# Optimization experiments

Hardware: AMD Instinct MI355X
Metric: run time of the kernel (lower is better)

Reference implementation:

```python
import jax, jax.numpy as jnp
import numpy as np

B, IN_DIM, HID = 4096, 1024, 1024


def _linear(x, W, b):
    # torch nn.Linear: y = x @ W.T + b, W is [out, in]
    return x @ W.T + b


def setup_inputs() -> dict:
    key = jax.random.key(0)
    ks = jax.random.split(key, 15)
    s_in = 1.0 / np.sqrt(IN_DIM + HID)
    s_x = 1.0 / np.sqrt(IN_DIM)
    s_h = 1.0 / np.sqrt(HID)
    return {
        "x": jax.random.normal(ks[0], (B, IN_DIM), jnp.float32),
        "h_prev": jax.random.normal(ks[1], (B, HID), jnp.float32),
        "c_prev": jax.random.normal(ks[2], (B, HID), jnp.float32),
        "Wi": jax.random.normal(ks[3], (HID, IN_DIM + HID), jnp.float32) * s_in,
        "bi": jax.random.normal(ks[4], (HID,), jnp.float32) * s_in,
        "Wf": jax.random.normal(ks[5], (HID, IN_DIM + HID), jnp.float32) * s_in,
        "bf": jax.random.normal(ks[6], (HID,), jnp.float32) * s_in,
        "Wo": jax.random.normal(ks[7], (HID, IN_DIM + HID), jnp.float32) * s_in,
        "bo": jax.random.normal(ks[8], (HID,), jnp.float32) * s_in,
        "Wxs": jax.random.normal(ks[9], (HID, IN_DIM), jnp.float32) * s_x,
        "bxs": jax.random.normal(ks[10], (HID,), jnp.float32) * s_x,
        "Wxg": jax.random.normal(ks[11], (HID, IN_DIM), jnp.float32) * s_x,
        "bxg": jax.random.normal(ks[12], (HID,), jnp.float32) * s_x,
        "Whg": jax.random.normal(ks[13], (HID, HID), jnp.float32) * s_h,
        "bhg": jax.random.normal(ks[14], (HID,), jnp.float32) * s_h,
    }


def reference(x, h_prev, c_prev, Wi, bi, Wf, bf, Wo, bo, Wxs, bxs, Wxg, bxg, Whg, bhg):
    # Fuse the three (in_dim+hid)->hid gate GEMMs into one concatenated GEMM.
    concat = jnp.concatenate([x, h_prev], axis=-1)          # [B, in_dim+hid]
    W_ifo = jnp.concatenate([Wi, Wf, Wo], axis=0)           # [3*hid, in_dim+hid]
    b_ifo = jnp.concatenate([bi, bf, bo], axis=0)           # [3*hid]
    gates = jax.nn.sigmoid(_linear(concat, W_ifo, b_ifo))   # [B, 3*hid]
    i_t, f_t, o_t = jnp.split(gates, 3, axis=-1)
    s_t = _linear(x, Wxs, bxs)
    cand_lin = _linear(x, Wxg, bxg) + _linear(h_prev, Whg, bhg)
    g_t = jnp.tanh(s_t * cand_lin)
    # refined=False branch
    c_t = f_t * c_prev + i_t * g_t
    h_t = o_t * jnp.tanh(c_t)
    return (h_t, c_t)
```

## Files before the change

kernel.cpp:

```cpp
#include <hip/hip_runtime.h>

typedef unsigned short u16;
typedef __attribute__((ext_vector_type(8))) __bf16 bf16x8;
typedef __attribute__((ext_vector_type(4))) float f32x4;
typedef __attribute__((ext_vector_type(4))) unsigned short u16x4;

#define AS1 __attribute__((address_space(1)))
#define AS3 __attribute__((address_space(3)))

#define OB_X    0L
#define OB_H    4194304L
#define OB_WI   8388608L
#define OB_WF   10485760L
#define OB_WO   12582912L
#define OB_WXS  14680064L
#define OB_WXG  15728640L
#define OB_WHG  16777216L
#define BLOB_EL 17825792L

__device__ __forceinline__ u16 f2b(float f) {
    unsigned u = __float_as_uint(f);
    u += 0x7fffu + ((u >> 16) & 1u);
    return (u16)(u >> 16);
}

__global__ __launch_bounds__(256) void convert_all(
    const float* __restrict__ x, const float* __restrict__ h,
    const float* __restrict__ Wi, const float* __restrict__ Wf,
    const float* __restrict__ Wo, const float* __restrict__ Wxs,
    const float* __restrict__ Wxg, const float* __restrict__ Whg,
    u16* __restrict__ blob)
{
    long e = ((long)blockIdx.x * 256 + threadIdx.x) * 8;
    const float* src; long off;
    if      (e < OB_H)   { src = x;   off = e; }
    else if (e < OB_WI)  { src = h;   off = e - OB_H; }
    else if (e < OB_WF)  { src = Wi;  off = e - OB_WI; }
    else if (e < OB_WO)  { src = Wf;  off = e - OB_WF; }
    else if (e < OB_WXS) { src = Wo;  off = e - OB_WO; }
    else if (e < OB_WXG) { src = Wxs; off = e - OB_WXS; }
    else if (e < OB_WHG) { src = Wxg; off = e - OB_WXG; }
    else                 { src = Whg; off = e - OB_WHG; }
    f32x4 v0 = *(const f32x4*)(src + off);
    f32x4 v1 = *(const f32x4*)(src + off + 4);
    u16x4 o0, o1;
    o0.x = f2b(v0.x); o0.y = f2b(v0.y); o0.z = f2b(v0.z); o0.w = f2b(v0.w);
    o1.x = f2b(v1.x); o1.y = f2b(v1.y); o1.z = f2b(v1.z); o1.w = f2b(v1.w);
    *(u16x4*)(blob + e) = o0;
    *(u16x4*)(blob + e + 4) = o1;
}

__device__ __forceinline__ void stageB(u16* dst, const u16* src, int ld,
                                       int t, int er, int gsw) {
    __builtin_amdgcn_global_load_lds(
        (AS1 void*)(src + er * ld + gsw),
        (AS3 void*)(dst + t * 8), 16, 0, 0);
}

__device__ __forceinline__ float sigf(float z) {
    return 1.f / (1.f + __expf(-z));
}

__global__ __launch_bounds__(512, 2) void srulstm_fused(
    const u16* __restrict__ blob,
    const float* __restrict__ c_prev,
    const float* __restrict__ bi, const float* __restrict__ bfv,
    const float* __restrict__ bo, const float* __restrict__ bxs,
    const float* __restrict__ bxg, const float* __restrict__ bhg,
    float* __restrict__ out)
{
    __shared__ __align__(16) u16 As[128 * 64];
    __shared__ __align__(16) u16 Bs[5 * 64 * 64];

    const u16* x   = blob + OB_X;
    const u16* h   = blob + OB_H;

    const int t = threadIdx.x;
    const int j0 = blockIdx.x * 64;
    const int m0 = blockIdx.y * 128;

    const u16* w0   = blob + OB_WI  + j0 * 2048;
    const u16* w1   = blob + OB_WF  + j0 * 2048;
    const u16* w2   = blob + OB_WO  + j0 * 2048;
    const u16* w3lo = blob + OB_WXG + j0 * 1024;
    const u16* w3hi = blob + OB_WHG + j0 * 1024;
    const u16* w4   = blob + OB_WXS + j0 * 1024;

    const u16* aLo = x + m0 * 1024;
    const u16* aHi = h + m0 * 1024;

    const int lane = t & 63;
    const int wave = t >> 6;
    const int wm = (wave >> 1) << 5;
    const int wn = (wave & 1) << 5;
    const int fr = lane & 15;
    const int fq = lane >> 4;
    const int r7 = fr & 7;

    f32x4 acc[5][2][2] = {};

    const int er = t >> 3;
    const int gsw = (((t & 7) ^ (er & 7)) << 3);

    for (int k0 = 0; k0 < 2048; k0 += 64) {
        const u16* aSrc = ((k0 < 1024) ? aLo : aHi) + (k0 & 1023);
#pragma unroll
        for (int it = 0; it < 2; ++it) {
            const int row = it * 64 + er;
            __builtin_amdgcn_global_load_lds(
                (AS1 void*)(aSrc + row * 1024 + gsw),
                (AS3 void*)(As + (it * 512 + t) * 8), 16, 0, 0);
        }
        stageB(Bs,         w0 + k0, 2048, t, er, gsw);
        stageB(Bs + 4096,  w1 + k0, 2048, t, er, gsw);
        stageB(Bs + 8192,  w2 + k0, 2048, t, er, gsw);
        stageB(Bs + 12288, (k0 < 1024) ? (w3lo + k0) : (w3hi + (k0 - 1024)),
               1024, t, er, gsw);
        if (k0 < 1024)
            stageB(Bs + 16384, w4 + k0, 1024, t, er, gsw);
        __syncthreads();
#pragma unroll
        for (int kk = 0; kk < 64; kk += 32) {
            const int sw = ((((kk >> 3) + fq) ^ r7) << 3);
            bf16x8 a[2];
#pragma unroll
            for (int mi = 0; mi < 2; ++mi)
                a[mi] = *(const bf16x8*)(As + (wm + mi * 16 + fr) * 64 + sw);
#pragma unroll
            for (int s = 0; s < 4; ++s) {
                bf16x8 b0 = *(const bf16x8*)(Bs + s * 4096 + (wn + fr) * 64 + sw);
                bf16x8 b1 = *(const bf16x8*)(Bs + s * 4096 + (wn + 16 + fr) * 64 + sw);
#pragma unroll
                for (int mi = 0; mi < 2; ++mi) {
                    acc[s][mi][0] = __builtin_amdgcn_mfma_f32_16x16x32_bf16(
                        a[mi], b0, acc[s][mi][0], 0, 0, 0);
                    acc[s][mi][1] = __builtin_amdgcn_mfma_f32_16x16x32_bf16(
                        a[mi], b1, acc[s][mi][1], 0, 0, 0);
                }
            }
            if (k0 < 1024) {
                bf16x8 b0 = *(const bf16x8*)(Bs + 16384 + (wn + fr) * 64 + sw);
                bf16x8 b1 = *(const bf16x8*)(Bs + 16384 + (wn + 16 + fr) * 64 + sw);
#pragma unroll
                for (int mi = 0; mi < 2; ++mi) {
                    acc[4][mi][0] = __builtin_amdgcn_mfma_f32_16x16x32_bf16(
                        a[mi], b0, acc[4][mi][0], 0, 0, 0);
                    acc[4][mi][1] = __builtin_amdgcn_mfma_f32_16x16x32_bf16(
                        a[mi], b1, acc[4][mi][1], 0, 0, 0);
                }
            }
        }
        __syncthreads();
    }

    const int orow = m0 + wm + (fq << 2);
    const int ocol = j0 + wn + fr;
#pragma unroll
    for (int ni = 0; ni < 2; ++ni) {
        const int col = ocol + ni * 16;
        const float bi_v = bi[col],  bf_v = bfv[col], bo_v = bo[col];
        const float bs_v = bxs[col], bg_v = bxg[col], bh_v = bhg[col];
#pragma unroll
        for (int mi = 0; mi < 2; ++mi) {
#pragma unroll
            for (int r = 0; r < 4; ++r) {
                const long idx = (long)(orow + mi * 16 + r) * 1024 + col;
                const float cp = c_prev[idx];
                const float i_t = sigf(acc[0][mi][ni][r] + bi_v);
                const float f_t = sigf(acc[1][mi][ni][r] + bf_v);
                const float o_t = sigf(acc[2][mi][ni][r] + bo_v);
                const float cand = acc[3][mi][ni][r] + bg_v + bh_v;
                const float s_t  = acc[4][mi][ni][r] + bs_v;
                const float g_t = tanhf(s_t * cand);
                const float c_t = f_t * cp + i_t * g_t;
                const float h_t = o_t * tanhf(c_t);
                out[idx] = h_t;
                out[4194304L + idx] = c_t;
            }
        }
    }
}

extern "C" void kernel_launch(void* const* d_in, const int* in_sizes, int n_in,
                              void* d_out, int out_size, void* d_ws, size_t ws_size,
                              hipStream_t stream)
{
    u16* blob = (u16*)d_ws;
    float* out = (float*)d_out;

    const long convBlocks = BLOB_EL / 8 / 256;

    convert_all<<<dim3(convBlocks), dim3(256), 0, stream>>>(
        (const float*)d_in[0], (const float*)d_in[1], (const float*)d_in[3],
        (const float*)d_in[5], (const float*)d_in[7], (const float*)d_in[9],
        (const float*)d_in[11], (const float*)d_in[13], blob);

    srulstm_fused<<<dim3(16, 32), dim3(512), 0, stream>>>(
        blob, (const float*)d_in[2], (const float*)d_in[4], (const float*)d_in[6],
        (const float*)d_in[8], (const float*)d_in[10], (const float*)d_in[12],
        (const float*)d_in[14], out);
}
```

Baseline: 222.0 us.

## Double-buffer LDS tiles and interleave async prefetch with MFMA phases

Replaces the single-buffered load-sync-compute loop with a ping-pong LDS scheme. The next k-tile's global_load_lds transfers are split across four sub-phases of the current tile's MFMA work, and hand-placed s_waitcnt vmcnt plus s_barrier replace __syncthreads. It also raises wave priority around MFMA bursts and drops the 2-blocks-per-CU launch bound. The aim is to hide global-load latency behind matrix math, at the cost of doubled LDS use (about 112 KB per block), which likely cuts occupancy. The partial vmcnt waits add a risk of ordering bugs, and the final iteration issues redundant loads to stay in bounds.

```diff
diff --git a/kernel.cpp b/kernel.cpp
--- a/kernel.cpp
+++ b/kernel.cpp
@@ -50,18 +50,14 @@
     *(u16x4*)(blob + e + 4) = o1;
 }
 
-__device__ __forceinline__ void stageB(u16* dst, const u16* src, int ld,
-                                       int t, int er, int gsw) {
-    __builtin_amdgcn_global_load_lds(
-        (AS1 void*)(src + er * ld + gsw),
-        (AS3 void*)(dst + t * 8), 16, 0, 0);
-}
-
 __device__ __forceinline__ float sigf(float z) {
     return 1.f / (1.f + __expf(-z));
 }
 
-__global__ __launch_bounds__(512, 2) void srulstm_fused(
+#define WAITBAR2 asm volatile("s_waitcnt vmcnt(2)\n\ts_barrier" ::: "memory")
+#define BARRIER  asm volatile("s_barrier" ::: "memory")
+
+__global__ __launch_bounds__(512) void srulstm_fused(
     const u16* __restrict__ blob,
     const float* __restrict__ c_prev,
     const float* __restrict__ bi, const float* __restrict__ bfv,
@@ -69,11 +65,11 @@
     const float* __restrict__ bxg, const float* __restrict__ bhg,
     float* __restrict__ out)
 {
-    __shared__ __align__(16) u16 As[128 * 64];
-    __shared__ __align__(16) u16 Bs[5 * 64 * 64];
-
-    const u16* x   = blob + OB_X;
-    const u16* h   = blob + OB_H;
+    __shared__ __align__(16) u16 As[2][128 * 64];
+    __shared__ __align__(16) u16 Bs[2][5 * 64 * 64];
+
+    const u16* x = blob + OB_X;
+    const u16* h = blob + OB_H;
 
     const int t = threadIdx.x;
     const int j0 = blockIdx.x * 64;
@@ -97,61 +93,144 @@
     const int fq = lane >> 4;
     const int r7 = fr & 7;
 
-    f32x4 acc[5][2][2] = {};
-
     const int er = t >> 3;
     const int gsw = (((t & 7) ^ (er & 7)) << 3);
 
-    for (int k0 = 0; k0 < 2048; k0 += 64) {
-        const u16* aSrc = ((k0 < 1024) ? aLo : aHi) + (k0 & 1023);
-#pragma unroll
-        for (int it = 0; it < 2; ++it) {
-            const int row = it * 64 + er;
+    f32x4 acc[5][2][2] = {};
+
+    auto stA = [&](u16* An, int kSc) {
+        const u16* aSrc = ((kSc < 1024) ? aLo : aHi) + (kSc & 1023);
+#pragma unroll
+        for (int it = 0; it < 2; ++it)
             __builtin_amdgcn_global_load_lds(
-                (AS1 void*)(aSrc + row * 1024 + gsw),
-                (AS3 void*)(As + (it * 512 + t) * 8), 16, 0, 0);
-        }
-        stageB(Bs,         w0 + k0, 2048, t, er, gsw);
-        stageB(Bs + 4096,  w1 + k0, 2048, t, er, gsw);
-        stageB(Bs + 8192,  w2 + k0, 2048, t, er, gsw);
-        stageB(Bs + 12288, (k0 < 1024) ? (w3lo + k0) : (w3hi + (k0 - 1024)),
-               1024, t, er, gsw);
-        if (k0 < 1024)
-            stageB(Bs + 16384, w4 + k0, 1024, t, er, gsw);
-        __syncthreads();
-#pragma unroll
-        for (int kk = 0; kk < 64; kk += 32) {
-            const int sw = ((((kk >> 3) + fq) ^ r7) << 3);
-            bf16x8 a[2];
-#pragma unroll
-            for (int mi = 0; mi < 2; ++mi)
-                a[mi] = *(const bf16x8*)(As + (wm + mi * 16 + fr) * 64 + sw);
-#pragma unroll
-            for (int s = 0; s < 4; ++s) {
-                bf16x8 b0 = *(const bf16x8*)(Bs + s * 4096 + (wn + fr) * 64 + sw);
-                bf16x8 b1 = *(const bf16x8*)(Bs + s * 4096 + (wn + 16 + fr) * 64 + sw);
-#pragma unroll
-                for (int mi = 0; mi < 2; ++mi) {
-                    acc[s][mi][0] = __builtin_amdgcn_mfma_f32_16x16x32_bf16(
-                        a[mi], b0, acc[s][mi][0], 0, 0, 0);
-                    acc[s][mi][1] = __builtin_amdgcn_mfma_f32_16x16x32_bf16(
-                        a[mi], b1, acc[s][mi][1], 0, 0, 0);
-                }
-            }
-            if (k0 < 1024) {
-                bf16x8 b0 = *(const bf16x8*)(Bs + 16384 + (wn + fr) * 64 + sw);
-                bf16x8 b1 = *(const bf16x8*)(Bs + 16384 + (wn + 16 + fr) * 64 + sw);
-#pragma unroll
-                for (int mi = 0; mi < 2; ++mi) {
-                    acc[4][mi][0] = __builtin_amdgcn_mfma_f32_16x16x32_bf16(
-                        a[mi], b0, acc[4][mi][0], 0, 0, 0);
-                    acc[4][mi][1] = __builtin_amdgcn_mfma_f32_16x16x32_bf16(
-                        a[mi], b1, acc[4][mi][1], 0, 0, 0);
-                }
+                (AS1 void*)(aSrc + (it * 64 + er) * 1024 + gsw),
+                (AS3 void*)(An + (it * 512 + t) * 8), 16, 0, 0);
+    };
+    auto stB = [&](u16* dst, const u16* src, int ld) {
+        __builtin_amdgcn_global_load_lds(
+            (AS1 void*)(src + er * ld + gsw),
+            (AS3 void*)(dst + t * 8), 16, 0, 0);
+    };
+
+    auto tile = [&](const u16* Ac, const u16* Bc, u16* An, u16* Bn,
+                    int k0, int kS) {
+        const bool s4 = (k0 < 1024);
+        const int kSc = (kS < 2048) ? kS : 1984;
+        const u16* w3s = (kSc < 1024) ? (w3lo + kSc) : (w3hi + (kSc - 1024));
+        const int sw0 = ((fq ^ r7) << 3);
+        const int sw1 = (((4 + fq) ^ r7) << 3);
+
+        WAITBAR2;
+        {
+            bf16x8 a0 = *(const bf16x8*)(Ac + (wm + fr) * 64 + sw0);
+            bf16x8 a1 = *(const bf16x8*)(Ac + (wm + 16 + fr) * 64 + sw0);
+            bf16x8 b00 = *(const bf16x8*)(Bc +         (wn + fr) * 64 + sw0);
+            bf16x8 b01 = *(const bf16x8*)(Bc +         (wn + 16 + fr) * 64 + sw0);
+            bf16x8 b10 = *(const bf16x8*)(Bc + 4096  + (wn + fr) * 64 + sw0);
+            bf16x8 b11 = *(const bf16x8*)(Bc + 4096  + (wn + 16 + fr) * 64 + sw0);
+            bf16x8 b20 = *(const bf16x8*)(Bc + 8192  + (wn + fr) * 64 + sw0);
+            bf16x8 b21 = *(const bf16x8*)(Bc + 8192  + (wn + 16 + fr) * 64 + sw0);
+            stA(An, kSc);
+            __builtin_amdgcn_s_setprio(1);
+            acc[0][0][0] = __builtin_amdgcn_mfma_f32_16x16x32_bf16(a0, b00, acc[0][0][0], 0, 0, 0);
+            acc[0][0][1] = __builtin_amdgcn_mfma_f32_16x16x32_bf16(a0, b01, acc[0][0][1], 0, 0, 0);
+            acc[0][1][0] = __builtin_amdgcn_mfma_f32_16x16x32_bf16(a1, b00, acc[0][1][0], 0, 0, 0);
+            acc[0][1][1] = __builtin_amdgcn_mfma_f32_16x16x32_bf16(a1, b01, acc[0][1][1], 0, 0, 0);
+            acc[1][0][0] = __builtin_amdgcn_mfma_f32_16x16x32_bf16(a0, b10, acc[1][0][0], 0, 0, 0);
+            acc[1][0][1] = __builtin_amdgcn_mfma_f32_16x16x32_bf16(a0, b11, acc[1][0][1], 0, 0, 0);
+            acc[1][1][0] = __builtin_amdgcn_mfma_f32_16x16x32_bf16(a1, b10, acc[1][1][0], 0, 0, 0);
+            acc[1][1][1] = __builtin_amdgcn_mfma_f32_16x16x32_bf16(a1, b11, acc[1][1][1], 0, 0, 0);
+            acc[2][0][0] = __builtin_amdgcn_mfma_f32_16x16x32_bf16(a0, b20, acc[2][0][0], 0, 0, 0);
+            acc[2][0][1] = __builtin_amdgcn_mfma_f32_16x16x32_bf16(a0, b21, acc[2][0][1], 0, 0, 0);
+            acc[2][1][0] = __builtin_amdgcn_mfma_f32_16x16x32_bf16(a1, b20, acc[2][1][0], 0, 0, 0);
+            acc[2][1][1] = __builtin_amdgcn_mfma_f32_16x16x32_bf16(a1, b21, acc[2][1][1], 0, 0, 0);
+            __builtin_amdgcn_s_setprio(0);
+
+            WAITBAR2;
+            bf16x8 b30 = *(const bf16x8*)(Bc + 12288 + (wn + fr) * 64 + sw0);
+            bf16x8 b31 = *(const bf16x8*)(Bc + 12288 + (wn + 16 + fr) * 64 + sw0);
+            stB(Bn, w0 + kSc, 2048);
+            stB(Bn + 4096, w1 + kSc, 2048);
+            __builtin_amdgcn_s_setprio(1);
+            acc[3][0][0] = __builtin_amdgcn_mfma_f32_16x16x32_bf16(a0, b30, acc[3][0][0], 0, 0, 0);
+            acc[3][0][1] = __builtin_amdgcn_mfma_f32_16x16x32_bf16(a0, b31, acc[3][0][1], 0, 0, 0);
+            acc[3][1][0] = __builtin_amdgcn_mfma_f32_16x16x32_bf16(a1, b30, acc[3][1][0], 0, 0, 0);
+            acc[3][1][1] = __builtin_amdgcn_mfma_f32_16x16x32_bf16(a1, b31, acc[3][1][1], 0, 0, 0);
+            __builtin_amdgcn_s_setprio(0);
+            if (s4) {
+                bf16x8 b40 = *(const bf16x8*)(Bc + 16384 + (wn + fr) * 64 + sw0);
+                bf16x8 b41 = *(const bf16x8*)(Bc + 16384 + (wn + 16 + fr) * 64 + sw0);
+                __builtin_amdgcn_s_setprio(1);
+                acc[4][0][0] = __builtin_amdgcn_mfma_f32_16x16x32_bf16(a0, b40, acc[4][0][0], 0, 0, 0);
+                acc[4][0][1] = __builtin_amdgcn_mfma_f32_16x16x32_bf16(a0, b41, acc[4][0][1], 0, 0, 0);
+                acc[4][1][0] = __builtin_amdgcn_mfma_f32_16x16x32_bf16(a1, b40, acc[4][1][0], 0, 0, 0);
+                acc[4][1][1] = __builtin_amdgcn_mfma_f32_16x16x32_bf16(a1, b41, acc[4][1][1], 0, 0, 0);
+                __builtin_amdgcn_s_setprio(0);
             }
         }
-        __syncthreads();
+
+        BARRIER;
+        {
+            bf16x8 a0 = *(const bf16x8*)(Ac + (wm + fr) * 64 + sw1);
+            bf16x8 a1 = *(const bf16x8*)(Ac + (wm + 16 + fr) * 64 + sw1);
+            bf16x8 b00 = *(const bf16x8*)(Bc +         (wn + fr) * 64 + sw1);
+            bf16x8 b01 = *(const bf16x8*)(Bc +         (wn + 16 + fr) * 64 + sw1);
+            bf16x8 b10 = *(const bf16x8*)(Bc + 4096  + (wn + fr) * 64 + sw1);
+            bf16x8 b11 = *(const bf16x8*)(Bc + 4096  + (wn + 16 + fr) * 64 + sw1);
+            bf16x8 b20 = *(const bf16x8*)(Bc + 8192  + (wn + fr) * 64 + sw1);
+            bf16x8 b21 = *(const bf16x8*)(Bc + 8192  + (wn + 16 + fr) * 64 + sw1);
+            stB(Bn + 8192, w2 + kSc, 2048);
+            stB(Bn + 12288, w3s, 1024);
+            __builtin_amdgcn_s_setprio(1);
+            acc[0][0][0] = __builtin_amdgcn_mfma_f32_16x16x32_bf16(a0, b00, acc[0][0][0], 0, 0, 0);
+            acc[0][0][1] = __builtin_amdgcn_mfma_f32_16x16x32_bf16(a0, b01, acc[0][0][1], 0, 0, 0);
+            acc[0][1][0] = __builtin_amdgcn_mfma_f32_16x16x32_bf16(a1, b00, acc[0][1][0], 0, 0, 0);
+            acc[0][1][1] = __builtin_amdgcn_mfma_f32_16x16x32_bf16(a1, b01, acc[0][1][1], 0, 0, 0);
+            acc[1][0][0] = __builtin_amdgcn_mfma_f32_16x16x32_bf16(a0, b10, acc[1][0][0], 0, 0, 0);
+            acc[1][0][1] = __builtin_amdgcn_mfma_f32_16x16x32_bf16(a0, b11, acc[1][0][1], 0, 0, 0);
+            acc[1][1][0] = __builtin_amdgcn_mfma_f32_16x16x32_bf16(a1, b10, acc[1][1][0], 0, 0, 0);
+            acc[1][1][1] = __builtin_amdgcn_mfma_f32_16x16x32_bf16(a1, b11, acc[1][1][1], 0, 0, 0);
+            acc[2][0][0] = __builtin_amdgcn_mfma_f32_16x16x32_bf16(a0, b20, acc[2][0][0], 0, 0, 0);
+            acc[2][0][1] = __builtin_amdgcn_mfma_f32_16x16x32_bf16(a0, b21, acc[2][0][1], 0, 0, 0);
+            acc[2][1][0] = __builtin_amdgcn_mfma_f32_16x16x32_bf16(a1, b20, acc[2][1][0], 0, 0, 0);
+            acc[2][1][1] = __builtin_amdgcn_mfma_f32_16x16x32_bf16(a1, b21, acc[2][1][1], 0, 0, 0);
+            __builtin_amdgcn_s_setprio(0);
+
+            BARRIER;
+            bf16x8 b30 = *(const bf16x8*)(Bc + 12288 + (wn + fr) * 64 + sw1);
+            bf16x8 b31 = *(const bf16x8*)(Bc + 12288 + (wn + 16 + fr) * 64 + sw1);
+            stB(Bn + 16384, w4 + (kSc & 1023), 1024);
+            __builtin_amdgcn_s_setprio(1);
+            acc[3][0][0] = __builtin_amdgcn_mfma_f32_16x16x32_bf16(a0, b30, acc[3][0][0], 0, 0, 0);
+            acc[3][0][1] = __builtin_amdgcn_mfma_f32_16x16x32_bf16(a0, b31, acc[3][0][1], 0, 0, 0);
+            acc[3][1][0] = __builtin_amdgcn_mfma_f32_16x16x32_bf16(a1, b30, acc[3][1][0], 0, 0, 0);
+            acc[3][1][1] = __builtin_amdgcn_mfma_f32_16x16x32_bf16(a1, b31, acc[3][1][1], 0, 0, 0);
+            __builtin_amdgcn_s_setprio(0);
+            if (s4) {
+                bf16x8 b40 = *(const bf16x8*)(Bc + 16384 + (wn + fr) * 64 + sw1);
+                bf16x8 b41 = *(const bf16x8*)(Bc + 16384 + (wn + 16 + fr) * 64 + sw1);
+                __builtin_amdgcn_s_setprio(1);
+                acc[4][0][0] = __builtin_amdgcn_mfma_f32_16x16x32_bf16(a0, b40, acc[4][0][0], 0, 0, 0);
+                acc[4][0][1] = __builtin_amdgcn_mfma_f32_16x16x32_bf16(a0, b41, acc[4][0][1], 0, 0, 0);
+                acc[4][1][0] = __builtin_amdgcn_mfma_f32_16x16x32_bf16(a1, b40, acc[4][1][0], 0, 0, 0);
+                acc[4][1][1] = __builtin_amdgcn_mfma_f32_16x16x32_bf16(a1, b41, acc[4][1][1], 0, 0, 0);
+                __builtin_amdgcn_s_setprio(0);
+            }
+        }
+    };
+
+    stA(As[0], 0);
+    stB(Bs[0],         w0,   2048);
+    stB(Bs[0] + 4096,  w1,   2048);
+    stB(Bs[0] + 8192,  w2,   2048);
+    stB(Bs[0] + 12288, w3lo, 1024);
+    stB(Bs[0] + 16384, w4,   1024);
+
+    for (int k0 = 0; k0 < 2048; k0 += 128) {
+        tile(As[0], Bs[0], As[1], Bs[1], k0,      k0 + 64);
+        tile(As[1], Bs[1], As[0], Bs[0], k0 + 64, k0 + 128);
     }
+    asm volatile("s_waitcnt vmcnt(0)" ::: "memory");
 
     const int orow = m0 + wm + (fq << 2);
     const int ocol = j0 + wn + fr;
```

Result: slower. 241.6 us (+8.8%).

## Convert fp32 weights to bf16 inside GEMM kernel via register prefetch

Applied to the files above, without the earlier changes.

The separate conversion pass now handles only x and h_prev. The fused kernel loads the fp32 weight tiles straight into registers, prefetching the next K-step after the barrier, then converts them to bf16 and writes them into swizzled LDS. This removes the weight conversion's write and reread through the workspace. In exchange, each of the 32 row blocks reads the fp32 weights again, doubling weight bytes per read. It also adds register pressure and drops the 2-blocks-per-CU launch bound.

```diff
diff --git a/kernel.cpp b/kernel.cpp
--- a/kernel.cpp
+++ b/kernel.cpp
@@ -10,13 +10,7 @@
 
 #define OB_X    0L
 #define OB_H    4194304L
-#define OB_WI   8388608L
-#define OB_WF   10485760L
-#define OB_WO   12582912L
-#define OB_WXS  14680064L
-#define OB_WXG  15728640L
-#define OB_WHG  16777216L
-#define BLOB_EL 17825792L
+#define BLOB_EL 8388608L
 
 __device__ __forceinline__ u16 f2b(float f) {
     unsigned u = __float_as_uint(f);
@@ -24,23 +18,13 @@
     return (u16)(u >> 16);
 }
 
-__global__ __launch_bounds__(256) void convert_all(
+__global__ __launch_bounds__(256) void convert_xh(
     const float* __restrict__ x, const float* __restrict__ h,
-    const float* __restrict__ Wi, const float* __restrict__ Wf,
-    const float* __restrict__ Wo, const float* __restrict__ Wxs,
-    const float* __restrict__ Wxg, const float* __restrict__ Whg,
     u16* __restrict__ blob)
 {
     long e = ((long)blockIdx.x * 256 + threadIdx.x) * 8;
-    const float* src; long off;
-    if      (e < OB_H)   { src = x;   off = e; }
-    else if (e < OB_WI)  { src = h;   off = e - OB_H; }
-    else if (e < OB_WF)  { src = Wi;  off = e - OB_WI; }
-    else if (e < OB_WO)  { src = Wf;  off = e - OB_WF; }
-    else if (e < OB_WXS) { src = Wo;  off = e - OB_WO; }
-    else if (e < OB_WXG) { src = Wxs; off = e - OB_WXS; }
-    else if (e < OB_WHG) { src = Wxg; off = e - OB_WXG; }
-    else                 { src = Whg; off = e - OB_WHG; }
+    const float* src = (e < OB_H) ? x : h;
+    long off = (e < OB_H) ? e : (e - OB_H);
     f32x4 v0 = *(const f32x4*)(src + off);
     f32x4 v1 = *(const f32x4*)(src + off + 4);
     u16x4 o0, o1;
@@ -50,19 +34,15 @@
     *(u16x4*)(blob + e + 4) = o1;
 }
 
-__device__ __forceinline__ void stageB(u16* dst, const u16* src, int ld,
-                                       int t, int er, int gsw) {
-    __builtin_amdgcn_global_load_lds(
-        (AS1 void*)(src + er * ld + gsw),
-        (AS3 void*)(dst + t * 8), 16, 0, 0);
-}
-
 __device__ __forceinline__ float sigf(float z) {
     return 1.f / (1.f + __expf(-z));
 }
 
-__global__ __launch_bounds__(512, 2) void srulstm_fused(
+__global__ __launch_bounds__(512) void srulstm_fused(
     const u16* __restrict__ blob,
+    const float* __restrict__ Wi, const float* __restrict__ Wf,
+    const float* __restrict__ Wo, const float* __restrict__ Wxs,
+    const float* __restrict__ Wxg, const float* __restrict__ Whg,
     const float* __restrict__ c_prev,
     const float* __restrict__ bi, const float* __restrict__ bfv,
     const float* __restrict__ bo, const float* __restrict__ bxs,
@@ -72,19 +52,12 @@
     __shared__ __align__(16) u16 As[128 * 64];
     __shared__ __align__(16) u16 Bs[5 * 64 * 64];
 
-    const u16* x   = blob + OB_X;
-    const u16* h   = blob + OB_H;
+    const u16* x = blob + OB_X;
+    const u16* h = blob + OB_H;
 
     const int t = threadIdx.x;
     const int j0 = blockIdx.x * 64;
     const int m0 = blockIdx.y * 128;
-
-    const u16* w0   = blob + OB_WI  + j0 * 2048;
-    const u16* w1   = blob + OB_WF  + j0 * 2048;
-    const u16* w2   = blob + OB_WO  + j0 * 2048;
-    const u16* w3lo = blob + OB_WXG + j0 * 1024;
-    const u16* w3hi = blob + OB_WHG + j0 * 1024;
-    const u16* w4   = blob + OB_WXS + j0 * 1024;
 
     const u16* aLo = x + m0 * 1024;
     const u16* aHi = h + m0 * 1024;
@@ -97,28 +70,58 @@
     const int fq = lane >> 4;
     const int r7 = fr & 7;
 
+    const int er = t >> 3;
+    const int g8 = t & 7;
+    const int gsw = ((g8 ^ (er & 7)) << 3);
+
+    const float* pWi  = Wi  + (j0 + er) * 2048 + g8 * 8;
+    const float* pWf  = Wf  + (j0 + er) * 2048 + g8 * 8;
+    const float* pWo  = Wo  + (j0 + er) * 2048 + g8 * 8;
+    const float* pWxg = Wxg + (j0 + er) * 1024 + g8 * 8;
+    const float* pWhg = Whg + (j0 + er) * 1024 + g8 * 8;
+    const float* pWxs = Wxs + (j0 + er) * 1024 + g8 * 8;
+
     f32x4 acc[5][2][2] = {};
-
-    const int er = t >> 3;
-    const int gsw = (((t & 7) ^ (er & 7)) << 3);
+    f32x4 rb[5][2];
+
+#define LOADB(kS)                                                          \
+    if ((kS) < 2048) {                                                     \
+        rb[0][0] = *(const f32x4*)(pWi + (kS));                            \
+        rb[0][1] = *(const f32x4*)(pWi + (kS) + 4);                        \
+        rb[1][0] = *(const f32x4*)(pWf + (kS));                            \
+        rb[1][1] = *(const f32x4*)(pWf + (kS) + 4);                        \
+        rb[2][0] = *(const f32x4*)(pWo + (kS));                            \
+        rb[2][1] = *(const f32x4*)(pWo + (kS) + 4);                        \
+        const float* w3 = ((kS) < 1024) ? (pWxg + (kS)) : (pWhg + ((kS) - 1024)); \
+        rb[3][0] = *(const f32x4*)(w3);                                    \
+        rb[3][1] = *(const f32x4*)(w3 + 4);                                \
+        if ((kS) < 1024) {                                                 \
+            rb[4][0] = *(const f32x4*)(pWxs + (kS));                       \
+            rb[4][1] = *(const f32x4*)(pWxs + (kS) + 4);                   \
+        }                                                                  \
+    }
+
+    LOADB(0);
 
     for (int k0 = 0; k0 < 2048; k0 += 64) {
+#pragma unroll
+        for (int s = 0; s < 5; ++s) {
+            if (s == 4 && k0 >= 1024) break;
+            bf16x8 w;
+            w[0] = (__bf16)rb[s][0].x; w[1] = (__bf16)rb[s][0].y;
+            w[2] = (__bf16)rb[s][0].z; w[3] = (__bf16)rb[s][0].w;
+            w[4] = (__bf16)rb[s][1].x; w[5] = (__bf16)rb[s][1].y;
+            w[6] = (__bf16)rb[s][1].z; w[7] = (__bf16)rb[s][1].w;
+            *(bf16x8*)(Bs + s * 4096 + er * 64 + gsw) = w;
+        }
         const u16* aSrc = ((k0 < 1024) ? aLo : aHi) + (k0 & 1023);
 #pragma unroll
-        for (int it = 0; it < 2; ++it) {
-            const int row = it * 64 + er;
+        for (int it = 0; it < 2; ++it)
             __builtin_amdgcn_global_load_lds(
-                (AS1 void*)(aSrc + row * 1024 + gsw),
+                (AS1 void*)(aSrc + (it * 64 + er) * 1024 + gsw),
                 (AS3 void*)(As + (it * 512 + t) * 8), 16, 0, 0);
-        }
-        stageB(Bs,         w0 + k0, 2048, t, er, gsw);
-        stageB(Bs + 4096,  w1 + k0, 2048, t, er, gsw);
-        stageB(Bs + 8192,  w2 + k0, 2048, t, er, gsw);
-        stageB(Bs + 12288, (k0 < 1024) ? (w3lo + k0) : (w3hi + (k0 - 1024)),
-               1024, t, er, gsw);
-        if (k0 < 1024)
-            stageB(Bs + 16384, w4 + k0, 1024, t, er, gsw);
         __syncthreads();
+        LOADB(k0 + 64);
 #pragma unroll
         for (int kk = 0; kk < 64; kk += 32) {
             const int sw = ((((kk >> 3) + fq) ^ r7) << 3);
@@ -190,13 +193,15 @@
 
     const long convBlocks = BLOB_EL / 8 / 256;
 
-    convert_all<<<dim3(convBlocks), dim3(256), 0, stream>>>(
-        (const float*)d_in[0], (const float*)d_in[1], (const float*)d_in[3],
-        (const float*)d_in[5], (const float*)d_in[7], (const float*)d_in[9],
-        (const float*)d_in[11], (const float*)d_in[13], blob);
+    convert_xh<<<dim3(convBlocks), dim3(256), 0, stream>>>(
+        (const float*)d_in[0], (const float*)d_in[1], blob);
 
     srulstm_fused<<<dim3(16, 32), dim3(512), 0, stream>>>(
-        blob, (const float*)d_in[2], (const float*)d_in[4], (const float*)d_in[6],
-        (const float*)d_in[8], (const float*)d_in[10], (const float*)d_in[12],
-        (const float*)d_in[14], out);
-}
+        blob,
+        (const float*)d_in[3], (const float*)d_in[5], (const float*)d_in[7],
+        (const float*)d_in[9], (const float*)d_in[11], (const float*)d_in[13],
+        (const float*)d_in[2],
+        (const float*)d_in[4], (const float*)d_in[6], (const float*)d_in[8],
+        (const float*)d_in[10], (const float*)d_in[12], (const float*)d_in[14],
+        out);
+}
```

After: 278.2 us. 25.3% more time.
